# Optimization experiments

Measured on AMD Instinct MI355X. Metric: run time of the kernel, lower is better.

Reference implementation:

```python
import jax, jax.numpy as jnp
import numpy as np

E = 8  # num_experts
K = 2  # top-k


def setup_inputs() -> dict:
    key = jax.random.key(0)
    k1, k2, k3, k4 = jax.random.split(key, 4)
    B, S, D, H = 4, 2048, 2048, 1024  # H = feed_forward // num_experts
    x = jax.random.normal(k1, (B, S, D), dtype=jnp.float32)
    Wg = jax.random.normal(k2, (D, E), dtype=jnp.float32) * 0.02
    W1 = jax.random.normal(k3, (E, D, H), dtype=jnp.float32) * 0.02
    W2 = jax.random.normal(k4, (E, H, D), dtype=jnp.float32) * 0.02
    return {"x": x, "Wg": Wg, "W1": W1, "W2": W2}


def reference(x, Wg, W1, W2):
    B, S, D = x.shape
    xf = x.reshape(-1, D)  # [N, D]
    gates = jax.nn.softmax(xf @ Wg, axis=-1)  # [N, E]
    topk_w, topk_i = jax.lax.top_k(gates, K)  # [N, K]
    # combine[n, e] = sum_k topk_w[n,k] * (topk_i[n,k] == e); zero for unselected experts
    combine = jnp.einsum("nk,nke->ne", topk_w,
                         jax.nn.one_hot(topk_i, E, dtype=gates.dtype))
    out = jnp.zeros_like(xf)
    for e in range(E):  # fixed small expert loop
        h = jax.nn.silu(xf @ W1[e])        # [N, H]
        y = h @ W2[e]                       # [N, D]
        out = out + combine[:, e:e + 1] * y
    # load-balancing loss: cv^2 of mean gate probs
    expert_probs = gates.mean(axis=0)
    m = expert_probs.mean()
    var = ((expert_probs - m) ** 2).mean()
    loss = var / (m ** 2 + 1e-10)
    return out.reshape(B, S, D), loss
```

## Files before the change

kernel.cpp:

```cpp
#include <hip/hip_runtime.h>
#include <hip/hip_bf16.h>

typedef _Float16 f16;
typedef _Float16 f16x4 __attribute__((ext_vector_type(4)));
typedef _Float16 f16x8 __attribute__((ext_vector_type(8)));
typedef float f32x4 __attribute__((ext_vector_type(4)));

#define N_TOK  8192
#define DMODEL 2048
#define HDIM   1024
#define NEXP   8
#define MAX_ROWS 17408
#define ROW_TILES 136

__device__ inline void gload16(const void* g, void* l) {
    __builtin_amdgcn_global_load_lds((const __attribute__((address_space(1))) void*)g,
                                     (__attribute__((address_space(3))) void*)l, 16, 0, 0);
}

union PrepSm {
    float wg[NEXP][DMODEL];
    float t[4][64][65];
};

__device__ inline void transpose_body(
    int e, int c0, int r0, int tid, float (*t)[65],
    const float* __restrict__ W, f16* __restrict__ Wt, int R, int C)
{
    const float* Wm = W + (size_t)e * R * C;
    f16* Wo = Wt + (size_t)e * R * C;

    const int rr4 = tid >> 4, c4 = (tid & 15) * 4;
    #pragma unroll
    for (int i = 0; i < 4; ++i) {
        int r = rr4 + i * 16;
        float4 v = *(const float4*)(Wm + (size_t)(r0 + r) * C + c0 + c4);
        t[r][c4] = v.x; t[r][c4 + 1] = v.y; t[r][c4 + 2] = v.z; t[r][c4 + 3] = v.w;
    }
    __syncthreads();

    const int cc8 = tid >> 3, r8 = (tid & 7) * 8;
    #pragma unroll
    for (int i = 0; i < 2; ++i) {
        int cc = cc8 + i * 32;
        f16x8 h;
        #pragma unroll
        for (int q = 0; q < 8; ++q) h[q] = (f16)t[r8 + q][cc];
        *(f16x8*)(Wo + (size_t)(c0 + cc) * R + r0 + r8) = h;
    }
}

__global__ __launch_bounds__(1024) void prep_k(
    const float* __restrict__ x, const float* __restrict__ Wg,
    const float* __restrict__ W1, const float* __restrict__ W2,
    f16* __restrict__ x16, f16* __restrict__ W1t, f16* __restrict__ W2t,
    int* __restrict__ ch_e, float* __restrict__ ch_w, float* __restrict__ gates_out)
{
    __shared__ PrepSm sm;
    const int b = blockIdx.x, tid = threadIdx.x;

    if (b < 512) {
        #pragma unroll
        for (int it = 0; it < 4; ++it) {
            int f = it * 1024 + tid;
            int k = f >> 1, e0 = (f & 1) * 4;
            float4 v = *(const float4*)(Wg + (size_t)f * 4);
            sm.wg[e0][k] = v.x; sm.wg[e0 + 1][k] = v.y;
            sm.wg[e0 + 2][k] = v.z; sm.wg[e0 + 3][k] = v.w;
        }
        __syncthreads();

        const int wv = tid >> 6, ln = tid & 63;
        const int token = b * 16 + wv;
        const long rowb = (long)token * DMODEL;

        double acc[NEXP] = {};
        #pragma unroll
        for (int t = 0; t < 8; ++t) {
            const int v4 = t * 64 + ln;
            float4 a = *(const float4*)(x + rowb + (size_t)v4 * 4);
            f16x4 h; h[0] = (f16)a.x; h[1] = (f16)a.y; h[2] = (f16)a.z; h[3] = (f16)a.w;
            *(f16x4*)(x16 + rowb + (size_t)v4 * 4) = h;
            float xs[4] = {a.x, a.y, a.z, a.w};
            #pragma unroll
            for (int e = 0; e < NEXP; ++e) {
                float4 w = *(const float4*)&sm.wg[e][v4 * 4];
                acc[e] += (double)xs[0] * w.x + (double)xs[1] * w.y
                        + (double)xs[2] * w.z + (double)xs[3] * w.w;
            }
        }
        #pragma unroll
        for (int e = 0; e < NEXP; ++e) {
            double v = acc[e];
            #pragma unroll
            for (int s = 32; s; s >>= 1) v += __shfl_xor(v, s);
            acc[e] = v;
        }
        if (ln == 0) {
            int e0 = 0;
            #pragma unroll
            for (int e = 1; e < NEXP; ++e) if (acc[e] > acc[e0]) e0 = e;
            int e1 = (e0 == 0) ? 1 : 0;
            #pragma unroll
            for (int e = 0; e < NEXP; ++e) if (e != e0 && acc[e] > acc[e1]) e1 = e;
            float mx = (float)acc[e0];
            float g[NEXP], s = 0.f;
            #pragma unroll
            for (int e = 0; e < NEXP; ++e) { g[e] = __expf((float)acc[e] - mx); s += g[e]; }
            float inv = 1.f / s;
            #pragma unroll
            for (int e = 0; e < NEXP; ++e) g[e] *= inv;
            ch_e[token * 2] = e0; ch_e[token * 2 + 1] = e1;
            ch_w[token * 2] = g[e0]; ch_w[token * 2 + 1] = g[e1];
            float4 g0 = {g[0], g[1], g[2], g[3]}, g1 = {g[4], g[5], g[6], g[7]};
            *(float4*)(gates_out + (size_t)token * 8) = g0;
            *(float4*)(gates_out + (size_t)token * 8 + 4) = g1;
        }
    } else if (b < 1536) {
        const int g = (b - 512) * 4 + (tid >> 8);
        const int e = g >> 9, rem = g & 511;
        const int c0 = (rem & 15) * 64, r0 = (rem >> 4) * 64;
        transpose_body(e, c0, r0, tid & 255, sm.t[tid >> 8], W1, W1t, DMODEL, HDIM);
    } else {
        const int g = (b - 1536) * 4 + (tid >> 8);
        const int e = g >> 9, rem = g & 511;
        const int c0 = (rem & 31) * 64, r0 = (rem >> 5) * 64;
        transpose_body(e, c0, r0, tid & 255, sm.t[tid >> 8], W2, W2t, HDIM, DMODEL);
    }
}

#define TPB_R 1024
#define TOK_T 8
__global__ __launch_bounds__(TPB_R) void route_k(
    const int* __restrict__ ch_e, const float* __restrict__ gates,
    int* __restrict__ poff, int* __restrict__ tok_list, int* __restrict__ pair_list,
    float* __restrict__ loss_out)
{
    __shared__ int scnt[TPB_R][NEXP];
    __shared__ int lpoff[NEXP + 1];
    __shared__ int ltot[NEXP];
    __shared__ float redl[16][NEXP];

    const int t = threadIdx.x;
    const int wv = t >> 6, ln = t & 63;

    int es[TOK_T * 2];
    #pragma unroll
    for (int i = 0; i < TOK_T; ++i) {
        int2 ee = *(const int2*)(ch_e + (size_t)(t * TOK_T + i) * 2);
        es[2 * i] = ee.x; es[2 * i + 1] = ee.y;
    }
    float lsum[NEXP] = {};
    #pragma unroll
    for (int i = 0; i < TOK_T; ++i) {
        const float4* gp = (const float4*)(gates + (size_t)(t * TOK_T + i) * 8);
        float4 a = gp[0], b = gp[1];
        lsum[0] += a.x; lsum[1] += a.y; lsum[2] += a.z; lsum[3] += a.w;
        lsum[4] += b.x; lsum[5] += b.y; lsum[6] += b.z; lsum[7] += b.w;
    }
    #pragma unroll
    for (int e = 0; e < NEXP; ++e) {
        int c = 0;
        #pragma unroll
        for (int i = 0; i < TOK_T * 2; ++i) c += (es[i] == e);
        scnt[t][e] = c;
        float v = lsum[e];
        #pragma unroll
        for (int s = 32; s; s >>= 1) v += __shfl_xor(v, s);
        lsum[e] = v;
    }
    if (ln == 0) {
        #pragma unroll
        for (int e = 0; e < NEXP; ++e) redl[wv][e] = lsum[e];
    }
    __syncthreads();

    if (wv < NEXP) {
        const int e = wv;
        int run = 0;
        #pragma unroll
        for (int i = 0; i < 16; ++i) {
            int idx = ln * 16 + i;
            int tmp = scnt[idx][e];
            scnt[idx][e] = run;
            run += tmp;
        }
        int incl = run;
        #pragma unroll
        for (int s = 1; s < 64; s <<= 1) {
            int v = __shfl_up(incl, s);
            if (ln >= s) incl += v;
        }
        int excl = incl - run;
        #pragma unroll
        for (int i = 0; i < 16; ++i) scnt[ln * 16 + i][e] += excl;
        if (ln == 63) ltot[e] = incl;
    }
    __syncthreads();
    if (t == 0) {
        int off = 0;
        #pragma unroll
        for (int e = 0; e < NEXP; ++e) { lpoff[e] = off; poff[e] = off; off += ((ltot[e] + 127) & ~127); }
        lpoff[NEXP] = off; poff[NEXP] = off;
        float ep[NEXP];
        #pragma unroll
        for (int e = 0; e < NEXP; ++e) {
            float s = 0.f;
            for (int w = 0; w < 16; ++w) s += redl[w][e];
            ep[e] = s * (1.f / (float)N_TOK);
        }
        float m = 0.f;
        #pragma unroll
        for (int e = 0; e < NEXP; ++e) m += ep[e];
        m *= (1.f / NEXP);
        float var = 0.f;
        #pragma unroll
        for (int e = 0; e < NEXP; ++e) { float d = ep[e] - m; var += d * d; }
        var *= (1.f / NEXP);
        loss_out[0] = var / (m * m + 1e-10f);
    }
    __syncthreads();

    #pragma unroll
    for (int i = 0; i < TOK_T * 2; ++i) {
        int e = es[i];
        int rank = 0;
        #pragma unroll
        for (int j = 0; j < i; ++j) rank += (es[j] == e);
        int row = lpoff[e] + scnt[t][e] + rank;
        int n = t * TOK_T + (i >> 1);
        tok_list[row] = n;
        pair_list[row] = n * 2 + (i & 1);
    }
}

template<bool G1>
__global__ __launch_bounds__(256, 3) void ggemm_k(
    const f16* __restrict__ A, const f16* __restrict__ Wt,
    const int* __restrict__ poff,
    const int* __restrict__ tok_list, const int* __restrict__ pair_list,
    f16* __restrict__ Hout, f16* __restrict__ Yp)
{
    constexpr int K   = G1 ? DMODEL : HDIM;
    constexpr int NJ  = G1 ? HDIM : DMODEL;
    constexpr int NCT = NJ / 128;

    __shared__ int s_off[NEXP + 1];
    __shared__ f16 lA[128 * 64];
    __shared__ f16 lB[128 * 64];

    if (threadIdx.x < NEXP + 1) s_off[threadIdx.x] = poff[threadIdx.x];
    __syncthreads();

    const int xcd = blockIdx.x & 7;
    const int i   = blockIdx.x >> 3;
    int rloc, ct;
    if (i < 12 * NCT) {
        const int g = i / (4 * NCT), r = i % (4 * NCT);
        rloc = g * 4 + (r & 3);
        ct   = r >> 2;
    } else {
        const int j = i - 12 * NCT;
        rloc = 12 + j % 5;
        ct   = j / 5;
    }
    const int rt = xcd * 17 + rloc;

    const int row0 = rt * 128;
    if (row0 >= s_off[NEXP]) return;
    int e = 0;
    #pragma unroll
    for (int ii = 0; ii < NEXP - 1; ++ii) if (row0 >= s_off[ii + 1]) e = ii + 1;

    const int wv = threadIdx.x >> 6, ln = threadIdx.x & 63;

    const int rbase = 32 * wv + (ln >> 3);
    const int c     = (ln & 7) ^ (ln >> 3);
    const f16* srcA[4];
    if (G1) {
        #pragma unroll
        for (int ii = 0; ii < 4; ++ii)
            srcA[ii] = A + (long)tok_list[row0 + rbase + 8 * ii] * DMODEL + c * 8;
    } else {
        srcA[0] = A + (long)(row0 + rbase) * HDIM + c * 8;
    }
    const f16* srcB = Wt + ((long)e * NJ + ct * 128 + rbase) * K + c * 8;

    f32x4 acc[4][4] = {};
    const int wr = wv >> 1, wc = wv & 1;
    const int l16 = ln & 15, lk = ln >> 4;

    for (int k0 = 0; k0 < K; k0 += 64) {
        #pragma unroll
        for (int ii = 0; ii < 4; ++ii) {
            const f16* sa = G1 ? (srcA[ii] + k0) : (srcA[0] + (size_t)(8 * ii) * K + k0);
            gload16(sa, &lA[(32 * wv + 8 * ii) * 64]);
            gload16(srcB + (size_t)(8 * ii) * K + k0, &lB[(32 * wv + 8 * ii) * 64]);
        }
        __syncthreads();
        #pragma unroll
        for (int kk = 0; kk < 2; ++kk) {
            f16x8 af[4], bf[4];
            #pragma unroll
            for (int m = 0; m < 4; ++m) {
                int r = wr * 64 + m * 16 + l16;
                int ch = (kk * 4 + lk) ^ (r & 7);
                af[m] = *(const f16x8*)&lA[r * 64 + ch * 8];
            }
            #pragma unroll
            for (int n = 0; n < 4; ++n) {
                int j = wc * 64 + n * 16 + l16;
                int ch = (kk * 4 + lk) ^ (j & 7);
                bf[n] = *(const f16x8*)&lB[j * 64 + ch * 8];
            }
            #pragma unroll
            for (int m = 0; m < 4; ++m)
                #pragma unroll
                for (int n = 0; n < 4; ++n)
                    acc[m][n] = __builtin_amdgcn_mfma_f32_16x16x32_f16(af[m], bf[n], acc[m][n], 0, 0, 0);
        }
        __syncthreads();
    }

    if (G1) {
        #pragma unroll
        for (int m = 0; m < 4; ++m) {
            int rb = row0 + wr * 64 + m * 16 + lk * 4;
            #pragma unroll
            for (int n = 0; n < 4; ++n) {
                int cc = ct * 128 + wc * 64 + n * 16 + l16;
                #pragma unroll
                for (int j2 = 0; j2 < 4; ++j2) {
                    float v = acc[m][n][j2];
                    v = v / (1.f + __expf(-v));
                    Hout[(long)(rb + j2) * HDIM + cc] = (f16)v;
                }
            }
        }
    } else {
        #pragma unroll
        for (int m = 0; m < 4; ++m) {
            int rb = row0 + wr * 64 + m * 16 + lk * 4;
            #pragma unroll
            for (int j2 = 0; j2 < 4; ++j2) {
                int p = pair_list[rb + j2];
                if (p >= 0) {
                    f16* yp = Yp + (long)p * DMODEL + ct * 128 + wc * 64 + l16;
                    #pragma unroll
                    for (int n = 0; n < 4; ++n)
                        yp[n * 16] = (f16)acc[m][n][j2];
                }
            }
        }
    }
}

__global__ __launch_bounds__(256) void combine_k(
    const f16* __restrict__ Yp, const float* __restrict__ ch_w,
    float* __restrict__ out)
{
    const int n = blockIdx.x, t = threadIdx.x;
    const float w0 = ch_w[n * 2], w1 = ch_w[n * 2 + 1];
    const f16x8 a = *(const f16x8*)(Yp + ((long)n * 2) * DMODEL + t * 8);
    const f16x8 b = *(const f16x8*)(Yp + ((long)n * 2 + 1) * DMODEL + t * 8);
    float4 o0, o1;
    o0.x = w0 * (float)a[0] + w1 * (float)b[0];
    o0.y = w0 * (float)a[1] + w1 * (float)b[1];
    o0.z = w0 * (float)a[2] + w1 * (float)b[2];
    o0.w = w0 * (float)a[3] + w1 * (float)b[3];
    o1.x = w0 * (float)a[4] + w1 * (float)b[4];
    o1.y = w0 * (float)a[5] + w1 * (float)b[5];
    o1.z = w0 * (float)a[6] + w1 * (float)b[6];
    o1.w = w0 * (float)a[7] + w1 * (float)b[7];
    float* op = out + (long)n * DMODEL + t * 8;
    *(float4*)op = o0;
    *(float4*)(op + 4) = o1;
}

extern "C" void kernel_launch(void* const* d_in, const int* in_sizes, int n_in,
                              void* d_out, int out_size, void* d_ws, size_t ws_size,
                              hipStream_t stream)
{
    const float* x  = (const float*)d_in[0];
    const float* Wg = (const float*)d_in[1];
    const float* W1 = (const float*)d_in[2];
    const float* W2 = (const float*)d_in[3];
    float* out = (float*)d_out;

    char* ws = (char*)d_ws;
    size_t o = 0;
    auto alloc = [&](size_t bytes) { size_t r = o; o = (o + bytes + 255) & ~(size_t)255; return r; };
    int*   poff      = (int*)(ws + alloc((NEXP + 1) * 4));
    float* gates     = (float*)(ws + alloc((size_t)N_TOK * NEXP * 4));
    int*   ch_e      = (int*)(ws + alloc((size_t)N_TOK * 2 * 4));
    float* ch_w      = (float*)(ws + alloc((size_t)N_TOK * 2 * 4));
    int*   tok_list  = (int*)(ws + alloc((size_t)MAX_ROWS * 4));
    int*   pair_list = (int*)(ws + alloc((size_t)MAX_ROWS * 4));
    f16*   x16       = (f16*)(ws + alloc((size_t)N_TOK * DMODEL * 2));
    f16*   W1t       = (f16*)(ws + alloc((size_t)NEXP * DMODEL * HDIM * 2));
    f16*   W2t       = (f16*)(ws + alloc((size_t)NEXP * DMODEL * HDIM * 2));
    f16*   hbuf      = (f16*)(ws + alloc((size_t)MAX_ROWS * HDIM * 2));
    f16*   Yp        = x16;
    (void)ws_size; (void)in_sizes; (void)n_in;

    hipMemsetAsync(tok_list, 0, (size_t)MAX_ROWS * 4, stream);
    hipMemsetAsync(pair_list, 0xFF, (size_t)MAX_ROWS * 4, stream);

    prep_k<<<2560, 1024, 0, stream>>>(x, Wg, W1, W2, x16, W1t, W2t, ch_e, ch_w, gates);
    route_k<<<1, TPB_R, 0, stream>>>(ch_e, gates, poff, tok_list, pair_list,
                                     out + (size_t)N_TOK * DMODEL);
    ggemm_k<true ><<<ROW_TILES * (HDIM / 128), 256, 0, stream>>>(x16, W1t, poff, tok_list, pair_list, hbuf, nullptr);
    ggemm_k<false><<<ROW_TILES * (DMODEL / 128), 256, 0, stream>>>(hbuf, W2t, poff, tok_list, pair_list, nullptr, Yp);
    combine_k<<<N_TOK, 256, 0, stream>>>(Yp, ch_w, out);
}
```

Baseline: 307.0 us.

## Move W2 transpose into the first grouped GEMM launch to overlap with compute

The fp32-to-fp16 transpose of W2 moves out of the prep kernel and into extra blocks appended to the first expert GEMM launch. That work can then overlap with the GEMM1 tiles instead of sitting on the critical path before routing. The gating path also now loads all x vectors up front before converting and accumulating, to expose more memory parallelism. The GEMM's shared memory becomes a union to hold the transpose tile, and the trailing transpose blocks may compete for CUs with the GEMM tiles.

```diff
diff --git a/kernel.cpp b/kernel.cpp
--- a/kernel.cpp
+++ b/kernel.cpp
@@ -18,42 +18,40 @@
                                      (__attribute__((address_space(3))) void*)l, 16, 0, 0);
 }
 
+__device__ inline void transpose_tile256(
+    int e, int c0, int r0, int tid, float (*t)[65],
+    const float* __restrict__ W, f16* __restrict__ Wt, int R, int C)
+{
+    const float* Wm = W + (size_t)e * R * C;
+    f16* Wo = Wt + (size_t)e * R * C;
+    const int rr4 = tid >> 4, c4 = (tid & 15) * 4;
+    #pragma unroll
+    for (int i = 0; i < 4; ++i) {
+        int r = rr4 + i * 16;
+        float4 v = *(const float4*)(Wm + (size_t)(r0 + r) * C + c0 + c4);
+        t[r][c4] = v.x; t[r][c4 + 1] = v.y; t[r][c4 + 2] = v.z; t[r][c4 + 3] = v.w;
+    }
+    __syncthreads();
+    const int cc8 = tid >> 3, r8 = (tid & 7) * 8;
+    #pragma unroll
+    for (int i = 0; i < 2; ++i) {
+        int cc = cc8 + i * 32;
+        f16x8 h;
+        #pragma unroll
+        for (int q = 0; q < 8; ++q) h[q] = (f16)t[r8 + q][cc];
+        *(f16x8*)(Wo + (size_t)(c0 + cc) * R + r0 + r8) = h;
+    }
+}
+
 union PrepSm {
     float wg[NEXP][DMODEL];
     float t[4][64][65];
 };
 
-__device__ inline void transpose_body(
-    int e, int c0, int r0, int tid, float (*t)[65],
-    const float* __restrict__ W, f16* __restrict__ Wt, int R, int C)
-{
-    const float* Wm = W + (size_t)e * R * C;
-    f16* Wo = Wt + (size_t)e * R * C;
-
-    const int rr4 = tid >> 4, c4 = (tid & 15) * 4;
-    #pragma unroll
-    for (int i = 0; i < 4; ++i) {
-        int r = rr4 + i * 16;
-        float4 v = *(const float4*)(Wm + (size_t)(r0 + r) * C + c0 + c4);
-        t[r][c4] = v.x; t[r][c4 + 1] = v.y; t[r][c4 + 2] = v.z; t[r][c4 + 3] = v.w;
-    }
-    __syncthreads();
-
-    const int cc8 = tid >> 3, r8 = (tid & 7) * 8;
-    #pragma unroll
-    for (int i = 0; i < 2; ++i) {
-        int cc = cc8 + i * 32;
-        f16x8 h;
-        #pragma unroll
-        for (int q = 0; q < 8; ++q) h[q] = (f16)t[r8 + q][cc];
-        *(f16x8*)(Wo + (size_t)(c0 + cc) * R + r0 + r8) = h;
-    }
-}
-
 __global__ __launch_bounds__(1024) void prep_k(
     const float* __restrict__ x, const float* __restrict__ Wg,
-    const float* __restrict__ W1, const float* __restrict__ W2,
-    f16* __restrict__ x16, f16* __restrict__ W1t, f16* __restrict__ W2t,
+    const float* __restrict__ W1,
+    f16* __restrict__ x16, f16* __restrict__ W1t,
     int* __restrict__ ch_e, float* __restrict__ ch_w, float* __restrict__ gates_out)
 {
     __shared__ PrepSm sm;
@@ -74,19 +72,27 @@
         const int token = b * 16 + wv;
         const long rowb = (long)token * DMODEL;
 
+        float4 xa[8];
+        #pragma unroll
+        for (int t = 0; t < 8; ++t)
+            xa[t] = *(const float4*)(x + rowb + (size_t)(t * 64 + ln) * 4);
+
+        #pragma unroll
+        for (int t = 0; t < 8; ++t) {
+            f16x4 h; h[0] = (f16)xa[t].x; h[1] = (f16)xa[t].y;
+            h[2] = (f16)xa[t].z; h[3] = (f16)xa[t].w;
+            *(f16x4*)(x16 + rowb + (size_t)(t * 64 + ln) * 4) = h;
+        }
+
         double acc[NEXP] = {};
         #pragma unroll
         for (int t = 0; t < 8; ++t) {
             const int v4 = t * 64 + ln;
-            float4 a = *(const float4*)(x + rowb + (size_t)v4 * 4);
-            f16x4 h; h[0] = (f16)a.x; h[1] = (f16)a.y; h[2] = (f16)a.z; h[3] = (f16)a.w;
-            *(f16x4*)(x16 + rowb + (size_t)v4 * 4) = h;
-            float xs[4] = {a.x, a.y, a.z, a.w};
             #pragma unroll
             for (int e = 0; e < NEXP; ++e) {
                 float4 w = *(const float4*)&sm.wg[e][v4 * 4];
-                acc[e] += (double)xs[0] * w.x + (double)xs[1] * w.y
-                        + (double)xs[2] * w.z + (double)xs[3] * w.w;
+                acc[e] += (double)xa[t].x * w.x + (double)xa[t].y * w.y
+                        + (double)xa[t].z * w.z + (double)xa[t].w * w.w;
             }
         }
         #pragma unroll
@@ -116,16 +122,11 @@
             *(float4*)(gates_out + (size_t)token * 8) = g0;
             *(float4*)(gates_out + (size_t)token * 8 + 4) = g1;
         }
-    } else if (b < 1536) {
+    } else {
         const int g = (b - 512) * 4 + (tid >> 8);
         const int e = g >> 9, rem = g & 511;
         const int c0 = (rem & 15) * 64, r0 = (rem >> 4) * 64;
-        transpose_body(e, c0, r0, tid & 255, sm.t[tid >> 8], W1, W1t, DMODEL, HDIM);
-    } else {
-        const int g = (b - 1536) * 4 + (tid >> 8);
-        const int e = g >> 9, rem = g & 511;
-        const int c0 = (rem & 31) * 64, r0 = (rem >> 5) * 64;
-        transpose_body(e, c0, r0, tid & 255, sm.t[tid >> 8], W2, W2t, HDIM, DMODEL);
+        transpose_tile256(e, c0, r0, tid & 255, sm.t[tid >> 8], W1, W1t, DMODEL, HDIM);
     }
 }
 
@@ -234,22 +235,34 @@
     }
 }
 
+union GemmSm {
+    struct { int s_off[NEXP + 1]; f16 lA[128 * 64]; f16 lB[128 * 64]; } g;
+    float t[64][65];
+};
+
 template<bool G1>
 __global__ __launch_bounds__(256, 3) void ggemm_k(
     const f16* __restrict__ A, const f16* __restrict__ Wt,
     const int* __restrict__ poff,
     const int* __restrict__ tok_list, const int* __restrict__ pair_list,
-    f16* __restrict__ Hout, f16* __restrict__ Yp)
+    f16* __restrict__ Hout, f16* __restrict__ Yp,
+    const float* __restrict__ W2, f16* __restrict__ W2t)
 {
     constexpr int K   = G1 ? DMODEL : HDIM;
     constexpr int NJ  = G1 ? HDIM : DMODEL;
     constexpr int NCT = NJ / 128;
 
-    __shared__ int s_off[NEXP + 1];
-    __shared__ f16 lA[128 * 64];
-    __shared__ f16 lB[128 * 64];
-
-    if (threadIdx.x < NEXP + 1) s_off[threadIdx.x] = poff[threadIdx.x];
+    __shared__ GemmSm sm;
+
+    if (G1 && blockIdx.x >= ROW_TILES * NCT) {
+        const int idx = blockIdx.x - ROW_TILES * NCT;
+        const int e = idx >> 9, rem = idx & 511;
+        const int c0 = (rem & 31) * 64, r0 = (rem >> 5) * 64;
+        transpose_tile256(e, c0, r0, threadIdx.x, sm.t, W2, W2t, HDIM, DMODEL);
+        return;
+    }
+
+    if (threadIdx.x < NEXP + 1) sm.g.s_off[threadIdx.x] = poff[threadIdx.x];
     __syncthreads();
 
     const int xcd = blockIdx.x & 7;
@@ -267,10 +280,10 @@
     const int rt = xcd * 17 + rloc;
 
     const int row0 = rt * 128;
-    if (row0 >= s_off[NEXP]) return;
+    if (row0 >= sm.g.s_off[NEXP]) return;
     int e = 0;
     #pragma unroll
-    for (int ii = 0; ii < NEXP - 1; ++ii) if (row0 >= s_off[ii + 1]) e = ii + 1;
+    for (int ii = 0; ii < NEXP - 1; ++ii) if (row0 >= sm.g.s_off[ii + 1]) e = ii + 1;
 
     const int wv = threadIdx.x >> 6, ln = threadIdx.x & 63;
 
@@ -294,8 +307,8 @@
         #pragma unroll
         for (int ii = 0; ii < 4; ++ii) {
             const f16* sa = G1 ? (srcA[ii] + k0) : (srcA[0] + (size_t)(8 * ii) * K + k0);
-            gload16(sa, &lA[(32 * wv + 8 * ii) * 64]);
-            gload16(srcB + (size_t)(8 * ii) * K + k0, &lB[(32 * wv + 8 * ii) * 64]);
+            gload16(sa, &sm.g.lA[(32 * wv + 8 * ii) * 64]);
+            gload16(srcB + (size_t)(8 * ii) * K + k0, &sm.g.lB[(32 * wv + 8 * ii) * 64]);
         }
         __syncthreads();
         #pragma unroll
@@ -305,13 +318,13 @@
             for (int m = 0; m < 4; ++m) {
                 int r = wr * 64 + m * 16 + l16;
                 int ch = (kk * 4 + lk) ^ (r & 7);
-                af[m] = *(const f16x8*)&lA[r * 64 + ch * 8];
+                af[m] = *(const f16x8*)&sm.g.lA[r * 64 + ch * 8];
             }
             #pragma unroll
             for (int n = 0; n < 4; ++n) {
                 int j = wc * 64 + n * 16 + l16;
                 int ch = (kk * 4 + lk) ^ (j & 7);
-                bf[n] = *(const f16x8*)&lB[j * 64 + ch * 8];
+                bf[n] = *(const f16x8*)&sm.g.lB[j * 64 + ch * 8];
             }
             #pragma unroll
             for (int m = 0; m < 4; ++m)
@@ -406,10 +419,12 @@
     hipMemsetAsync(tok_list, 0, (size_t)MAX_ROWS * 4, stream);
     hipMemsetAsync(pair_list, 0xFF, (size_t)MAX_ROWS * 4, stream);
 
-    prep_k<<<2560, 1024, 0, stream>>>(x, Wg, W1, W2, x16, W1t, W2t, ch_e, ch_w, gates);
+    prep_k<<<1536, 1024, 0, stream>>>(x, Wg, W1, x16, W1t, ch_e, ch_w, gates);
     route_k<<<1, TPB_R, 0, stream>>>(ch_e, gates, poff, tok_list, pair_list,
                                      out + (size_t)N_TOK * DMODEL);
-    ggemm_k<true ><<<ROW_TILES * (HDIM / 128), 256, 0, stream>>>(x16, W1t, poff, tok_list, pair_list, hbuf, nullptr);
-    ggemm_k<false><<<ROW_TILES * (DMODEL / 128), 256, 0, stream>>>(hbuf, W2t, poff, tok_list, pair_list, nullptr, Yp);
+    ggemm_k<true ><<<ROW_TILES * (HDIM / 128) + 4096, 256, 0, stream>>>(
+        x16, W1t, poff, tok_list, pair_list, hbuf, nullptr, W2, W2t);
+    ggemm_k<false><<<ROW_TILES * (DMODEL / 128), 256, 0, stream>>>(
+        hbuf, W2t, poff, tok_list, pair_list, nullptr, Yp, nullptr, nullptr);
     combine_k<<<N_TOK, 256, 0, stream>>>(Yp, ch_w, out);
 }
```

Result: slower. 440.7 us (+43.6%).

## Triple-buffer grouped GEMM with 128x256 tiles and 512-thread blocks

Applied to the files above, without the earlier changes.

Reworks the grouped expert GEMM to use 512-thread blocks computing 128x256 output tiles, with a three-slot LDS ring that prefetches two K-steps ahead via direct global-to-LDS loads. The single sync per K-step is replaced by split half-step barriers, explicit vmcnt waits and raised wave priority around the MFMA bursts. The goal is to hide global load latency behind matrix math and to reuse each A tile across a wider N span. In exchange it uses much more LDS (about 144KB), which lowers occupancy, and launches fewer blocks. The existing row-tile mapping may now leave part of the GPU idle.

```diff
diff --git a/kernel.cpp b/kernel.cpp
--- a/kernel.cpp
+++ b/kernel.cpp
@@ -29,7 +29,6 @@
 {
     const float* Wm = W + (size_t)e * R * C;
     f16* Wo = Wt + (size_t)e * R * C;
-
     const int rr4 = tid >> 4, c4 = (tid & 15) * 4;
     #pragma unroll
     for (int i = 0; i < 4; ++i) {
@@ -38,7 +37,6 @@
         t[r][c4] = v.x; t[r][c4 + 1] = v.y; t[r][c4 + 2] = v.z; t[r][c4 + 3] = v.w;
     }
     __syncthreads();
-
     const int cc8 = tid >> 3, r8 = (tid & 7) * 8;
     #pragma unroll
     for (int i = 0; i < 2; ++i) {
@@ -235,7 +233,7 @@
 }
 
 template<bool G1>
-__global__ __launch_bounds__(256, 3) void ggemm_k(
+__global__ __launch_bounds__(512) void ggemm_k(
     const f16* __restrict__ A, const f16* __restrict__ Wt,
     const int* __restrict__ poff,
     const int* __restrict__ tok_list, const int* __restrict__ pair_list,
@@ -243,11 +241,12 @@
 {
     constexpr int K   = G1 ? DMODEL : HDIM;
     constexpr int NJ  = G1 ? HDIM : DMODEL;
-    constexpr int NCT = NJ / 128;
-
+    constexpr int NCT = NJ / 256;
+    constexpr int NT  = K / 64;
+
+    __shared__ f16 sA[3][128 * 64];
+    __shared__ f16 sB[3][256 * 64];
     __shared__ int s_off[NEXP + 1];
-    __shared__ f16 lA[128 * 64];
-    __shared__ f16 lB[128 * 64];
 
     if (threadIdx.x < NEXP + 1) s_off[threadIdx.x] = poff[threadIdx.x];
     __syncthreads();
@@ -265,62 +264,95 @@
         ct   = j / 5;
     }
     const int rt = xcd * 17 + rloc;
-
     const int row0 = rt * 128;
     if (row0 >= s_off[NEXP]) return;
     int e = 0;
     #pragma unroll
     for (int ii = 0; ii < NEXP - 1; ++ii) if (row0 >= s_off[ii + 1]) e = ii + 1;
 
-    const int wv = threadIdx.x >> 6, ln = threadIdx.x & 63;
-
-    const int rbase = 32 * wv + (ln >> 3);
-    const int c     = (ln & 7) ^ (ln >> 3);
-    const f16* srcA[4];
+    const int t = threadIdx.x, wv = t >> 6, ln = t & 63;
+    const int lrow = ln >> 3;
+    const int c = (ln & 7) ^ lrow;
+
+    const f16* srcA[2];
     if (G1) {
-        #pragma unroll
-        for (int ii = 0; ii < 4; ++ii)
-            srcA[ii] = A + (long)tok_list[row0 + rbase + 8 * ii] * DMODEL + c * 8;
+        srcA[0] = A + (long)tok_list[row0 + wv * 8 + lrow] * DMODEL + c * 8;
+        srcA[1] = A + (long)tok_list[row0 + wv * 8 + lrow + 64] * DMODEL + c * 8;
     } else {
-        srcA[0] = A + (long)(row0 + rbase) * HDIM + c * 8;
-    }
-    const f16* srcB = Wt + ((long)e * NJ + ct * 128 + rbase) * K + c * 8;
+        srcA[0] = A + (long)(row0 + wv * 8 + lrow) * HDIM + c * 8;
+        srcA[1] = srcA[0] + (size_t)64 * HDIM;
+    }
+    const f16* srcB[4];
+    #pragma unroll
+    for (int bi = 0; bi < 4; ++bi)
+        srcB[bi] = Wt + ((long)e * NJ + ct * 256 + wv * 8 + lrow + 64 * bi) * K + c * 8;
+
+    #define STAGE_A(slot, kt, i_) gload16(srcA[i_] + (size_t)(kt) * 64, &sA[slot][(wv * 8 + 64 * (i_)) * 64])
+    #define STAGE_B(slot, kt, i_) gload16(srcB[i_] + (size_t)(kt) * 64, &sB[slot][(wv * 8 + 64 * (i_)) * 64])
 
     f32x4 acc[4][4] = {};
-    const int wr = wv >> 1, wc = wv & 1;
+    const int wr = wv >> 2, wc = wv & 3;
     const int l16 = ln & 15, lk = ln >> 4;
-
-    for (int k0 = 0; k0 < K; k0 += 64) {
-        #pragma unroll
-        for (int ii = 0; ii < 4; ++ii) {
-            const f16* sa = G1 ? (srcA[ii] + k0) : (srcA[0] + (size_t)(8 * ii) * K + k0);
-            gload16(sa, &lA[(32 * wv + 8 * ii) * 64]);
-            gload16(srcB + (size_t)(8 * ii) * K + k0, &lB[(32 * wv + 8 * ii) * 64]);
-        }
-        __syncthreads();
-        #pragma unroll
-        for (int kk = 0; kk < 2; ++kk) {
+    const int arow = wr * 64 + l16;
+    const int brow = wc * 64 + l16;
+
+    STAGE_A(0, 0, 0); STAGE_A(0, 0, 1);
+    STAGE_B(0, 0, 0); STAGE_B(0, 0, 1); STAGE_B(0, 0, 2); STAGE_B(0, 0, 3);
+    STAGE_A(1, 1, 0); STAGE_A(1, 1, 1);
+    STAGE_B(1, 1, 0); STAGE_B(1, 1, 1); STAGE_B(1, 1, 2); STAGE_B(1, 1, 3);
+    asm volatile("s_waitcnt vmcnt(6)" ::: "memory");
+    __builtin_amdgcn_s_barrier();
+
+    int slot = 0;
+    for (int kt = 0; kt < NT; ++kt) {
+        const int snext = (slot >= 1) ? slot - 1 : slot + 2;
+        const bool pf = (kt + 2 < NT);
+        {
+            const int ch = lk ^ (l16 & 7);
             f16x8 af[4], bf[4];
             #pragma unroll
-            for (int m = 0; m < 4; ++m) {
-                int r = wr * 64 + m * 16 + l16;
-                int ch = (kk * 4 + lk) ^ (r & 7);
-                af[m] = *(const f16x8*)&lA[r * 64 + ch * 8];
-            }
-            #pragma unroll
-            for (int n = 0; n < 4; ++n) {
-                int j = wc * 64 + n * 16 + l16;
-                int ch = (kk * 4 + lk) ^ (j & 7);
-                bf[n] = *(const f16x8*)&lB[j * 64 + ch * 8];
-            }
+            for (int m = 0; m < 4; ++m)
+                af[m] = *(const f16x8*)&sA[slot][(arow + m * 16) * 64 + ch * 8];
+            #pragma unroll
+            for (int n = 0; n < 4; ++n)
+                bf[n] = *(const f16x8*)&sB[slot][(brow + n * 16) * 64 + ch * 8];
+            if (pf) { STAGE_A(snext, kt + 2, 0); STAGE_A(snext, kt + 2, 1); STAGE_B(snext, kt + 2, 0); }
+            __builtin_amdgcn_s_barrier();
+            __builtin_amdgcn_s_setprio(1);
             #pragma unroll
             for (int m = 0; m < 4; ++m)
                 #pragma unroll
                 for (int n = 0; n < 4; ++n)
                     acc[m][n] = __builtin_amdgcn_mfma_f32_16x16x32_f16(af[m], bf[n], acc[m][n], 0, 0, 0);
-        }
-        __syncthreads();
-    }
+            __builtin_amdgcn_s_setprio(0);
+            __builtin_amdgcn_s_barrier();
+        }
+        {
+            const int ch = (4 + lk) ^ (l16 & 7);
+            f16x8 af[4], bf[4];
+            #pragma unroll
+            for (int m = 0; m < 4; ++m)
+                af[m] = *(const f16x8*)&sA[slot][(arow + m * 16) * 64 + ch * 8];
+            #pragma unroll
+            for (int n = 0; n < 4; ++n)
+                bf[n] = *(const f16x8*)&sB[slot][(brow + n * 16) * 64 + ch * 8];
+            if (pf) { STAGE_B(snext, kt + 2, 1); STAGE_B(snext, kt + 2, 2); STAGE_B(snext, kt + 2, 3); }
+            if (pf)                 asm volatile("s_waitcnt vmcnt(6)" ::: "memory");
+            else if (kt + 1 < NT)   asm volatile("s_waitcnt vmcnt(0)" ::: "memory");
+            __builtin_amdgcn_s_barrier();
+            __builtin_amdgcn_s_setprio(1);
+            #pragma unroll
+            for (int m = 0; m < 4; ++m)
+                #pragma unroll
+                for (int n = 0; n < 4; ++n)
+                    acc[m][n] = __builtin_amdgcn_mfma_f32_16x16x32_f16(af[m], bf[n], acc[m][n], 0, 0, 0);
+            __builtin_amdgcn_s_setprio(0);
+            __builtin_amdgcn_s_barrier();
+        }
+        slot = (slot == 2) ? 0 : slot + 1;
+    }
+    #undef STAGE_A
+    #undef STAGE_B
 
     if (G1) {
         #pragma unroll
@@ -328,7 +360,7 @@
             int rb = row0 + wr * 64 + m * 16 + lk * 4;
             #pragma unroll
             for (int n = 0; n < 4; ++n) {
-                int cc = ct * 128 + wc * 64 + n * 16 + l16;
+                int cc = ct * 256 + wc * 64 + n * 16 + l16;
                 #pragma unroll
                 for (int j2 = 0; j2 < 4; ++j2) {
                     float v = acc[m][n][j2];
@@ -345,7 +377,7 @@
             for (int j2 = 0; j2 < 4; ++j2) {
                 int p = pair_list[rb + j2];
                 if (p >= 0) {
-                    f16* yp = Yp + (long)p * DMODEL + ct * 128 + wc * 64 + l16;
+                    f16* yp = Yp + (long)p * DMODEL + ct * 256 + wc * 64 + l16;
                     #pragma unroll
                     for (int n = 0; n < 4; ++n)
                         yp[n * 16] = (f16)acc[m][n][j2];
@@ -409,7 +441,7 @@
     prep_k<<<2560, 1024, 0, stream>>>(x, Wg, W1, W2, x16, W1t, W2t, ch_e, ch_w, gates);
     route_k<<<1, TPB_R, 0, stream>>>(ch_e, gates, poff, tok_list, pair_list,
                                      out + (size_t)N_TOK * DMODEL);
-    ggemm_k<true ><<<ROW_TILES * (HDIM / 128), 256, 0, stream>>>(x16, W1t, poff, tok_list, pair_list, hbuf, nullptr);
-    ggemm_k<false><<<ROW_TILES * (DMODEL / 128), 256, 0, stream>>>(hbuf, W2t, poff, tok_list, pair_list, nullptr, Yp);
+    ggemm_k<true ><<<ROW_TILES * (HDIM / 256), 512, 0, stream>>>(x16, W1t, poff, tok_list, pair_list, hbuf, nullptr);
+    ggemm_k<false><<<ROW_TILES * (DMODEL / 256), 512, 0, stream>>>(hbuf, W2t, poff, tok_list, pair_list, nullptr, Yp);
     combine_k<<<N_TOK, 256, 0, stream>>>(Yp, ch_w, out);
 }
```

Measured after the change: 335.8 us. +9.4%, slower.
